# Optimization experiments

Hardware: AMD Instinct MI355X
Metric: run time of the kernel (lower is better)

Reference implementation:

```python
import jax, jax.numpy as jnp
import numpy as np


def _edge_softmax_by_src(e, src, n_nodes):
    # DGL edge_softmax(norm_by='src'): softmax over outgoing edges of each src node
    m = jax.ops.segment_max(e, src, num_segments=n_nodes)
    ex = jnp.exp(e - m[src])
    s = jax.ops.segment_sum(ex, src, num_segments=n_nodes)
    return ex / s[src]


def _l2norm(x):
    # F.normalize(p=2, dim=-1), eps=1e-12
    n = jnp.linalg.norm(x, axis=-1, keepdims=True)
    return x / jnp.maximum(n, 1e-12)


def setup_inputs() -> dict:
    key = jax.random.key(0)
    ks = jax.random.split(key, 16)
    N, E, D, NC = 50000, 1600000, 64, 16   # main graph nodes/edges, dim, classes
    NCL, ECL, FCL = 32, 1024, 16           # coarsened line graph: nodes=etypes
    s = 0.1
    inp = {
        "cl_h": jax.random.normal(ks[0], (NCL, FCL), jnp.float32),
        "cl_w": jax.random.normal(ks[1], (ECL,), jnp.float32),
        "cl_src": jax.random.randint(ks[2], (ECL,), 0, NCL, jnp.int32),
        "cl_dst": jax.random.randint(ks[3], (ECL,), 0, NCL, jnp.int32),
        "g_src": jax.random.randint(ks[4], (E,), 0, N, jnp.int32),
        "g_dst": jax.random.randint(ks[5], (E,), 0, N, jnp.int32),
        "g_etype": jax.random.randint(ks[6], (E,), 0, NCL, jnp.int32),
        # learned parameters
        "feats_emb": jax.random.normal(ks[7], (N, D), jnp.float32) * s,
        "W_e": jax.random.normal(ks[8], (FCL, D), jnp.float32) * s,      # linear_e (no bias)
        "beta1": jnp.array(1.0, jnp.float32),
        "eps1": jnp.array(0.0, jnp.float32),
        "beta2": jnp.array(1.0, jnp.float32),
        "eps2": jnp.array(0.0, jnp.float32),
        "W1a": jax.random.normal(ks[9], (D, D), jnp.float32) * s,
        "W2a": jax.random.normal(ks[10], (D, D), jnp.float32) * s,
        "W1b": jax.random.normal(ks[11], (D, D), jnp.float32) * s,
        "W2b": jax.random.normal(ks[12], (D, D), jnp.float32) * s,
        "W_pred": jax.random.normal(ks[13], (D, NC), jnp.float32) * s,
        "b_pred": jnp.zeros((NC,), jnp.float32),
    }
    return inp


def reference(cl_h, cl_w, cl_src, cl_dst, g_src, g_dst, g_etype,
              feats_emb, W_e, beta1, eps1, beta2, eps2,
              W1a, W2a, W1b, W2b, W_pred, b_pred):
    NCL = cl_h.shape[0]
    N = feats_emb.shape[0]

    def agnn(feat, beta, eps):
        p = _edge_softmax_by_src(beta * cl_w, cl_src, NCL)           # [Ecl]
        nh = _l2norm(feat)                                           # [NCL, F]
        agg = jax.ops.segment_sum(nh[cl_src] * p[:, None], cl_dst,
                                  num_segments=NCL)                  # [NCL, F]
        return (1.0 + eps) * feat + agg

    # edge-type feature propagation on coarsened line graph (dropout is eval-mode identity)
    h = jax.nn.relu(agnn(cl_h, beta1, eps1))
    h = jax.nn.relu(agnn(h, beta2, eps2))

    # per-edge relation embedding on main graph
    ew = h[g_etype] @ W_e                                            # [E, D]

    def gconv(feat, W1, W2):
        msg = feat[g_src] - ew                                       # u_sub_e, [E, D]
        agg = jax.ops.segment_sum(msg, g_dst, num_segments=N)        # [N, D]
        return jnp.tanh(feat @ W1 + agg @ W2)

    x = gconv(feats_emb, W1a, W2a)
    x = gconv(x, W1b, W2b)
    return x @ W_pred + b_pred
```

## Files before the change

### kernel.cpp

```cpp
#include <hip/hip_runtime.h>


#define TILE 8192

typedef __attribute__((ext_vector_type(8))) unsigned short us8;

__device__ __forceinline__ float b2f(unsigned short h) {
    return __uint_as_float(((unsigned)h) << 16);
}
__device__ __forceinline__ unsigned short f2b(float f) {
    const unsigned u = __float_as_uint(f);
    return (unsigned short)((u + 0x7FFFu + ((u >> 16) & 1u)) >> 16);
}

__device__ __forceinline__ unsigned ford_enc(float v) {
    unsigned b = __float_as_uint(v);
    return (b & 0x80000000u) ? ~b : (b | 0x80000000u);
}
__device__ __forceinline__ float ford_dec(unsigned k) {
    return __uint_as_float((k & 0x80000000u) ? (k ^ 0x80000000u) : ~k);
}

__global__ __launch_bounds__(512) void agnn_kernel(
    const float* __restrict__ cl_h, const float* __restrict__ cl_w,
    const int* __restrict__ cl_src, const int* __restrict__ cl_dst,
    const float* __restrict__ W_e,
    const float* __restrict__ pb1, const float* __restrict__ pe1,
    const float* __restrict__ pb2, const float* __restrict__ pe2,
    float* __restrict__ hW, int* __restrict__ bcnt, int ECL)
{
    __shared__ float w_s[1024];
    __shared__ int   src_s[1024];
    __shared__ int   dst_s[1024];
    __shared__ float h[32][16];
    __shared__ float nh[32][16];
    __shared__ float p[1024];
    __shared__ float red[32][16];
    __shared__ float acc16[32][16][16];
    __shared__ unsigned mI[32];
    __shared__ float m[32], ssum[32], nrm[32];
    const int tid = threadIdx.x;
    const int seg = tid >> 4, j = tid & 15;

    if (tid < 256) bcnt[tid] = 0;

    for (int e = tid; e < ECL; e += 512) {
        w_s[e] = cl_w[e]; src_s[e] = cl_src[e]; dst_s[e] = cl_dst[e];
    }
    h[tid >> 4][tid & 15] = cl_h[tid];
    __syncthreads();

    for (int layer = 0; layer < 2; ++layer) {
        const float beta = layer ? *pb2 : *pb1;
        const float eps  = layer ? *pe2 : *pe1;

        if (tid < 32) mI[tid] = ford_enc(-3.4e38f);
        __syncthreads();
        for (int e = tid; e < ECL; e += 512)
            atomicMax(&mI[src_s[e]], ford_enc(beta * w_s[e]));
        __syncthreads();
        if (tid < 32) m[tid] = ford_dec(mI[tid]);
        __syncthreads();

        for (int e = tid; e < ECL; e += 512)
            p[e] = __expf(beta * w_s[e] - m[src_s[e]]);
        __syncthreads();

        {
            float s = 0.f;
            #pragma unroll 4
            for (int e = j; e < ECL; e += 16)
                s += (src_s[e] == seg) ? p[e] : 0.f;
            red[seg][j] = s;
        }
        __syncthreads();
        if (tid < 32) {
            float s = 0.f;
            #pragma unroll
            for (int k = 0; k < 16; ++k) s += red[tid][k];
            ssum[tid] = s;
            float q = 0.f;
            #pragma unroll
            for (int f = 0; f < 16; ++f) { float v = h[tid][f]; q += v * v; }
            nrm[tid] = fmaxf(sqrtf(q), 1e-12f);
        }
        __syncthreads();
        for (int e = tid; e < ECL; e += 512)
            p[e] = p[e] / ssum[src_s[e]];
        nh[tid >> 4][tid & 15] = h[tid >> 4][tid & 15] / nrm[tid >> 4];
        __syncthreads();

        {
            float facc[16];
            #pragma unroll
            for (int f = 0; f < 16; ++f) facc[f] = 0.f;
            #pragma unroll 4
            for (int e = j; e < ECL; e += 16) {
                if (dst_s[e] == seg) {
                    const float pe = p[e];
                    const float4* nhrow = reinterpret_cast<const float4*>(&nh[src_s[e]][0]);
                    const float4 a0 = nhrow[0], a1 = nhrow[1], a2 = nhrow[2], a3 = nhrow[3];
                    facc[0] += pe * a0.x; facc[1] += pe * a0.y; facc[2] += pe * a0.z; facc[3] += pe * a0.w;
                    facc[4] += pe * a1.x; facc[5] += pe * a1.y; facc[6] += pe * a1.z; facc[7] += pe * a1.w;
                    facc[8] += pe * a2.x; facc[9] += pe * a2.y; facc[10] += pe * a2.z; facc[11] += pe * a2.w;
                    facc[12] += pe * a3.x; facc[13] += pe * a3.y; facc[14] += pe * a3.z; facc[15] += pe * a3.w;
                }
            }
            #pragma unroll
            for (int f = 0; f < 16; ++f) acc16[seg][j][f] = facc[f];
        }
        __syncthreads();
        {
            const int t = tid >> 4, f = tid & 15;
            float a = 0.f;
            #pragma unroll
            for (int k = 0; k < 16; ++k) a += acc16[t][k][f];
            float v = (1.f + eps) * h[t][f] + a;
            h[t][f] = fmaxf(v, 0.f);
        }
        __syncthreads();
    }

    for (int o = tid; o < 2048; o += 512) {
        const int t = o >> 6, d = o & 63;
        float s = 0.f;
        #pragma unroll
        for (int f = 0; f < 16; ++f) s += h[t][f] * W_e[f * 64 + d];
        hW[o] = s;
    }
}

__global__ __launch_bounds__(256) void tobf16_kernel(
    const float* __restrict__ x, unsigned short* __restrict__ y, int total8)
{
    const int i = blockIdx.x * 256 + threadIdx.x;
    if (i >= total8) return;
    const int base = i * 8;
    const float4 a = *reinterpret_cast<const float4*>(&x[base]);
    const float4 b = *reinterpret_cast<const float4*>(&x[base + 4]);
    us8 o;
    o[0] = f2b(a.x); o[1] = f2b(a.y); o[2] = f2b(a.z); o[3] = f2b(a.w);
    o[4] = f2b(b.x); o[5] = f2b(b.y); o[6] = f2b(b.z); o[7] = f2b(b.w);
    *reinterpret_cast<us8*>(&y[base]) = o;
}

__global__ __launch_bounds__(256) void bucket_count(
    const int* __restrict__ dst, int* __restrict__ bcnt, int E)
{
    __shared__ int lh[256];
    const int tid = threadIdx.x;
    lh[tid] = 0;
    __syncthreads();
    const int base = blockIdx.x * TILE;
    #pragma unroll
    for (int it = 0; it < 8; ++it) {
        const int i = base + (it * 256 + tid) * 4;
        if (i + 3 < E) {
            const int4 d = *reinterpret_cast<const int4*>(&dst[i]);
            atomicAdd(&lh[d.x >> 8], 1); atomicAdd(&lh[d.y >> 8], 1);
            atomicAdd(&lh[d.z >> 8], 1); atomicAdd(&lh[d.w >> 8], 1);
        } else {
            for (int k = i; k < E && k < i + 4; ++k) atomicAdd(&lh[dst[k] >> 8], 1);
        }
    }
    __syncthreads();
    if (lh[tid]) atomicAdd(&bcnt[tid], lh[tid]);
}

__global__ __launch_bounds__(256) void bucket_scan(
    const int* __restrict__ bcnt, int* __restrict__ bbase, int* __restrict__ bcur)
{
    __shared__ int ws[4];
    const int tid = threadIdx.x, lane = tid & 63, wv = tid >> 6;
    const int v = bcnt[tid];
    int x = v;
    #pragma unroll
    for (int s = 1; s < 64; s <<= 1) { const int t = __shfl_up(x, s, 64); if (lane >= s) x += t; }
    if (lane == 63) ws[wv] = x;
    __syncthreads();
    if (tid == 0) { int a = ws[0]; ws[0] = 0; for (int k = 1; k < 4; ++k) { const int b = ws[k]; ws[k] = a; a += b; } }
    __syncthreads();
    const int excl = ws[wv] + x - v;
    bbase[tid] = excl; bcur[tid] = excl;
    if (tid == 255) bbase[256] = excl + v;
}

__global__ __launch_bounds__(256) void bucket_scatter(
    const int* __restrict__ src, const int* __restrict__ dst, const int* __restrict__ et,
    int* __restrict__ bcur, unsigned* __restrict__ etmp, int E)
{
    __shared__ int lh[256], lofs[256], lcur[256], gbase[256];
    __shared__ int ws[4];
    __shared__ unsigned stage[TILE];
    __shared__ unsigned char sbk[TILE];
    const int tid = threadIdx.x, lane = tid & 63, wv = tid >> 6;
    lh[tid] = 0;
    __syncthreads();
    const int base = blockIdx.x * TILE;
    #pragma unroll
    for (int it = 0; it < 8; ++it) {
        const int i = base + (it * 256 + tid) * 4;
        if (i + 3 < E) {
            const int4 d = *reinterpret_cast<const int4*>(&dst[i]);
            atomicAdd(&lh[d.x >> 8], 1); atomicAdd(&lh[d.y >> 8], 1);
            atomicAdd(&lh[d.z >> 8], 1); atomicAdd(&lh[d.w >> 8], 1);
        } else {
            for (int k = i; k < E && k < i + 4; ++k) atomicAdd(&lh[dst[k] >> 8], 1);
        }
    }
    __syncthreads();
    {
        const int v = lh[tid];
        int x = v;
        #pragma unroll
        for (int s = 1; s < 64; s <<= 1) { const int t = __shfl_up(x, s, 64); if (lane >= s) x += t; }
        if (lane == 63) ws[wv] = x;
        __syncthreads();
        if (tid == 0) { int a = ws[0]; ws[0] = 0; for (int k = 1; k < 4; ++k) { const int b = ws[k]; ws[k] = a; a += b; } }
        __syncthreads();
        const int excl = ws[wv] + x - v;
        lofs[tid] = excl; lcur[tid] = excl;
        if (v) gbase[tid] = atomicAdd(&bcur[tid], v);
    }
    __syncthreads();
    #pragma unroll
    for (int it = 0; it < 8; ++it) {
        const int i = base + (it * 256 + tid) * 4;
        if (i + 3 < E) {
            const int4 d  = *reinterpret_cast<const int4*>(&dst[i]);
            const int4 s4 = *reinterpret_cast<const int4*>(&src[i]);
            const int4 t4 = *reinterpret_cast<const int4*>(&et[i]);
            int b, r;
            b = d.x >> 8; r = atomicAdd(&lcur[b], 1);
            stage[r] = (unsigned)s4.x | ((unsigned)(d.x & 255) << 16) | ((unsigned)t4.x << 24); sbk[r] = (unsigned char)b;
            b = d.y >> 8; r = atomicAdd(&lcur[b], 1);
            stage[r] = (unsigned)s4.y | ((unsigned)(d.y & 255) << 16) | ((unsigned)t4.y << 24); sbk[r] = (unsigned char)b;
            b = d.z >> 8; r = atomicAdd(&lcur[b], 1);
            stage[r] = (unsigned)s4.z | ((unsigned)(d.z & 255) << 16) | ((unsigned)t4.z << 24); sbk[r] = (unsigned char)b;
            b = d.w >> 8; r = atomicAdd(&lcur[b], 1);
            stage[r] = (unsigned)s4.w | ((unsigned)(d.w & 255) << 16) | ((unsigned)t4.w << 24); sbk[r] = (unsigned char)b;
        } else {
            for (int k = i; k < E && k < i + 4; ++k) {
                const int b = dst[k] >> 8;
                const int r = atomicAdd(&lcur[b], 1);
                stage[r] = (unsigned)src[k] | ((unsigned)(dst[k] & 255) << 16) | ((unsigned)et[k] << 24);
                sbk[r] = (unsigned char)b;
            }
        }
    }
    __syncthreads();
    const int tot = lofs[255] + lh[255];
    for (int i = tid; i < tot; i += 256) {
        const int b = sbk[i];
        etmp[gbase[b] + (i - lofs[b])] = stage[i];
    }
}

__global__ __launch_bounds__(256) void csr_kernel(
    const unsigned* __restrict__ etmp, const int* __restrict__ bbase,
    int* __restrict__ off, unsigned* __restrict__ ssrc, int N, int NB)
{
    __shared__ int lh[256], lofs[256], lcur[256];
    __shared__ int ws[4];
    const int tid = threadIdx.x, lane = tid & 63, wv = tid >> 6;
    const int b = blockIdx.x;
    const int s = bbase[b], e = bbase[b + 1];
    lh[tid] = 0;
    __syncthreads();
    for (int i = s + tid; i < e; i += 256)
        atomicAdd(&lh[(etmp[i] >> 16) & 255], 1);
    __syncthreads();
    {
        const int v = lh[tid];
        int x = v;
        #pragma unroll
        for (int ss = 1; ss < 64; ss <<= 1) { const int t = __shfl_up(x, ss, 64); if (lane >= ss) x += t; }
        if (lane == 63) ws[wv] = x;
        __syncthreads();
        if (tid == 0) { int a = ws[0]; ws[0] = 0; for (int k = 1; k < 4; ++k) { const int c = ws[k]; ws[k] = a; a += c; } }
        __syncthreads();
        const int excl = ws[wv] + x - v;
        lofs[tid] = excl; lcur[tid] = excl;
    }
    __syncthreads();
    const int n0 = b << 8;
    if (n0 + tid < N) off[n0 + tid] = s + lofs[tid];
    if (b == NB - 1 && tid == 0) off[N] = e;
    for (int i = s + tid; i < e; i += 256) {
        const unsigned pp = etmp[i];
        const int dl = (pp >> 16) & 255;
        const int r = atomicAdd(&lcur[dl], 1);
        ssrc[s + r] = pp;
    }
}

__global__ __launch_bounds__(256) void spmm_kernel(
    const unsigned short* __restrict__ fb, const float* __restrict__ hW,
    const int* __restrict__ off, const unsigned* __restrict__ ssrc,
    float* __restrict__ aggF, int N)
{
    __shared__ float hWl[2048];
    for (int i = threadIdx.x; i < 2048; i += 256) hWl[i] = hW[i];
    __syncthreads();
    const int lane = threadIdx.x & 63;
    const int n = blockIdx.x * 4 + (threadIdx.x >> 6);
    if (n >= N) return;
    const int half = lane >> 5, c = lane & 31;
    const int beg = off[n], end = off[n + 1];
    float a0 = 0.f, a1 = 0.f;
    int i = beg + half;
    for (; i + 14 < end; i += 16) {
        unsigned pp[8];
        #pragma unroll
        for (int jj = 0; jj < 8; ++jj) pp[jj] = ssrc[i + 2 * jj];
        unsigned u[8];
        #pragma unroll
        for (int jj = 0; jj < 8; ++jj)
            u[jj] = *reinterpret_cast<const unsigned*>(
                &fb[(size_t)(pp[jj] & 0xFFFFu) * 64 + 2 * c]);
        #pragma unroll
        for (int jj = 0; jj < 8; ++jj) {
            const float2 hw = *reinterpret_cast<const float2*>(
                &hWl[(pp[jj] >> 24) * 64 + 2 * c]);
            a0 += b2f((unsigned short)(u[jj] & 0xFFFFu)) - hw.x;
            a1 += b2f((unsigned short)(u[jj] >> 16)) - hw.y;
        }
    }
    for (; i + 6 < end; i += 8) {
        unsigned pp[4];
        #pragma unroll
        for (int jj = 0; jj < 4; ++jj) pp[jj] = ssrc[i + 2 * jj];
        unsigned u[4];
        #pragma unroll
        for (int jj = 0; jj < 4; ++jj)
            u[jj] = *reinterpret_cast<const unsigned*>(
                &fb[(size_t)(pp[jj] & 0xFFFFu) * 64 + 2 * c]);
        #pragma unroll
        for (int jj = 0; jj < 4; ++jj) {
            const float2 hw = *reinterpret_cast<const float2*>(
                &hWl[(pp[jj] >> 24) * 64 + 2 * c]);
            a0 += b2f((unsigned short)(u[jj] & 0xFFFFu)) - hw.x;
            a1 += b2f((unsigned short)(u[jj] >> 16)) - hw.y;
        }
    }
    for (; i < end; i += 2) {
        const unsigned pp = ssrc[i];
        const unsigned u = *reinterpret_cast<const unsigned*>(
            &fb[(size_t)(pp & 0xFFFFu) * 64 + 2 * c]);
        const float2 hw = *reinterpret_cast<const float2*>(
            &hWl[(pp >> 24) * 64 + 2 * c]);
        a0 += b2f((unsigned short)(u & 0xFFFFu)) - hw.x;
        a1 += b2f((unsigned short)(u >> 16)) - hw.y;
    }
    a0 += __shfl_xor(a0, 32);
    a1 += __shfl_xor(a1, 32);
    if (half == 0)
        *reinterpret_cast<float2*>(&aggF[(size_t)n * 64 + 2 * c]) = make_float2(a0, a1);
}

__global__ __launch_bounds__(256) void gconv_kernel(
    const float* __restrict__ Xf, const float* __restrict__ Af,
    const float* __restrict__ W1, const float* __restrict__ W2,
    float* __restrict__ x1f, unsigned short* __restrict__ out16,
    float* __restrict__ outf, int N, int final_mode,
    const float* __restrict__ Wp, const float* __restrict__ bp)
{
    __shared__ float4 fav[64 * 32];
    __shared__ float4 Wl[128 * 16];
    const int tid = threadIdx.x;
    const int ng = tid & 15, og = tid >> 4;
    const int n0 = blockIdx.x * 64;
    const int nb = ng * 4;

    #pragma unroll
    for (int q = 0; q < 8; ++q) {
        const int idx = q * 256 + tid;
        Wl[idx] = (idx < 1024)
            ? reinterpret_cast<const float4*>(W1)[idx]
            : reinterpret_cast<const float4*>(W2)[idx - 1024];
    }
    #pragma unroll
    for (int q = 0; q < 8; ++q) {
        const int cch = q * 256 + tid;
        const int row = cch >> 5, p = cch & 31;
        const int rn = n0 + row;
        float4 v = make_float4(0.f, 0.f, 0.f, 0.f);
        if (rn < N)
            v = (p < 16) ? reinterpret_cast<const float4*>(Xf)[(size_t)rn * 16 + p]
                         : reinterpret_cast<const float4*>(Af)[(size_t)rn * 16 + (p - 16)];
        fav[row * 32 + (p ^ ((row >> 2) & 7))] = v;
    }
    __syncthreads();

    float acc[4][4];
    #pragma unroll
    for (int i = 0; i < 4; ++i)
        #pragma unroll
        for (int j = 0; j < 4; ++j) acc[i][j] = 0.f;

    const int swz = ng & 7;
    #pragma unroll 2
    for (int kc = 0; kc < 32; ++kc) {
        const int pc = kc ^ swz;
        const float4 a0 = fav[(nb + 0) * 32 + pc];
        const float4 a1 = fav[(nb + 1) * 32 + pc];
        const float4 a2 = fav[(nb + 2) * 32 + pc];
        const float4 a3 = fav[(nb + 3) * 32 + pc];
        const float4 w0 = Wl[(kc * 4 + 0) * 16 + og];
        const float4 w1 = Wl[(kc * 4 + 1) * 16 + og];
        const float4 w2 = Wl[(kc * 4 + 2) * 16 + og];
        const float4 w3 = Wl[(kc * 4 + 3) * 16 + og];
        #pragma unroll
        for (int i = 0; i < 4; ++i) {
            const float4 a = (i == 0) ? a0 : (i == 1) ? a1 : (i == 2) ? a2 : a3;
            acc[i][0] += a.x * w0.x + a.y * w1.x + a.z * w2.x + a.w * w3.x;
            acc[i][1] += a.x * w0.y + a.y * w1.y + a.z * w2.y + a.w * w3.y;
            acc[i][2] += a.x * w0.z + a.y * w1.z + a.z * w2.z + a.w * w3.z;
            acc[i][3] += a.x * w0.w + a.y * w1.w + a.z * w2.w + a.w * w3.w;
        }
    }

    #pragma unroll
    for (int i = 0; i < 4; ++i)
        #pragma unroll
        for (int j = 0; j < 4; ++j) {
            const float e2 = __expf(2.f * acc[i][j]);
            acc[i][j] = 1.f - 2.f / (e2 + 1.f);
        }

    if (!final_mode) {
        #pragma unroll
        for (int i = 0; i < 4; ++i) {
            const int node = n0 + nb + i;
            if (node < N) {
                *reinterpret_cast<float4*>(&x1f[(size_t)node * 64 + og * 4]) =
                    make_float4(acc[i][0], acc[i][1], acc[i][2], acc[i][3]);
                const unsigned long long pk =
                    (unsigned long long)f2b(acc[i][0]) |
                    ((unsigned long long)f2b(acc[i][1]) << 16) |
                    ((unsigned long long)f2b(acc[i][2]) << 32) |
                    ((unsigned long long)f2b(acc[i][3]) << 48);
                *reinterpret_cast<unsigned long long*>(&out16[(size_t)node * 64 + og * 4]) = pk;
            }
        }
    } else {
        float* TL = reinterpret_cast<float*>(fav);
        __syncthreads();
        #pragma unroll
        for (int i = 0; i < 4; ++i)
            #pragma unroll
            for (int j = 0; j < 4; ++j)
                TL[(nb + i) * 65 + og * 4 + j] = acc[i][j];
        __syncthreads();
        const int l = tid & 63, cg = (tid >> 6) * 4;
        float o0 = bp[cg], o1 = bp[cg + 1], o2 = bp[cg + 2], o3 = bp[cg + 3];
        for (int d = 0; d < 64; ++d) {
            const float tv = TL[l * 65 + d];
            const float4 wp = *reinterpret_cast<const float4*>(&Wp[d * 16 + cg]);
            o0 += tv * wp.x; o1 += tv * wp.y; o2 += tv * wp.z; o3 += tv * wp.w;
        }
        const int node = n0 + l;
        if (node < N)
            *reinterpret_cast<float4*>(&outf[(size_t)node * 16 + cg]) =
                make_float4(o0, o1, o2, o3);
    }
}

extern "C" void kernel_launch(void* const* d_in, const int* in_sizes, int n_in,
                              void* d_out, int out_size, void* d_ws, size_t ws_size,
                              hipStream_t stream)
{
    const float* cl_h   = (const float*)d_in[0];
    const float* cl_w   = (const float*)d_in[1];
    const int*   cl_src = (const int*)d_in[2];
    const int*   cl_dst = (const int*)d_in[3];
    const int*   g_src  = (const int*)d_in[4];
    const int*   g_dst  = (const int*)d_in[5];
    const int*   g_et   = (const int*)d_in[6];
    const float* feats  = (const float*)d_in[7];
    const float* W_e    = (const float*)d_in[8];
    const float* b1     = (const float*)d_in[9];
    const float* e1     = (const float*)d_in[10];
    const float* b2     = (const float*)d_in[11];
    const float* e2     = (const float*)d_in[12];
    const float* W1a    = (const float*)d_in[13];
    const float* W2a    = (const float*)d_in[14];
    const float* W1b    = (const float*)d_in[15];
    const float* W2b    = (const float*)d_in[16];
    const float* Wp     = (const float*)d_in[17];
    const float* bp     = (const float*)d_in[18];
    const int ECL = in_sizes[1];
    const int E   = in_sizes[4];
    const int N   = in_sizes[7] / 64;
    const int NB  = (N + 255) >> 8;

    char* w = (char*)d_ws;
    auto carve = [&](size_t bytes) {
        char* r = w;
        w += (bytes + 255) & ~(size_t)255;
        return r;
    };
    float*          hW    = (float*)carve(32 * 64 * sizeof(float));
    int*            off   = (int*)carve((size_t)(N + 1) * sizeof(int));
    int*            bcnt  = (int*)carve(256 * sizeof(int));
    int*            bbase = (int*)carve(257 * sizeof(int));
    int*            bcur  = (int*)carve(256 * sizeof(int));
    unsigned*       etmp  = (unsigned*)carve((size_t)E * sizeof(unsigned));
    unsigned*       ssrc  = (unsigned*)carve((size_t)E * sizeof(unsigned));
    unsigned short* fb16  = (unsigned short*)carve((size_t)N * 64 * sizeof(unsigned short));
    unsigned short* x16   = (unsigned short*)carve((size_t)N * 64 * sizeof(unsigned short));
    float*          aggF  = (float*)carve((size_t)N * 64 * sizeof(float));
    float*          x1f   = (float*)carve((size_t)N * 64 * sizeof(float));

    const int nblk = (E + TILE - 1) / TILE;
    const int total8 = N * 8;

    agnn_kernel<<<1, 512, 0, stream>>>(cl_h, cl_w, cl_src, cl_dst, W_e,
                                       b1, e1, b2, e2, hW, bcnt, ECL);
    tobf16_kernel<<<(total8 + 255) / 256, 256, 0, stream>>>(feats, fb16, total8);
    bucket_count<<<nblk, 256, 0, stream>>>(g_dst, bcnt, E);
    bucket_scan<<<1, 256, 0, stream>>>(bcnt, bbase, bcur);
    bucket_scatter<<<nblk, 256, 0, stream>>>(g_src, g_dst, g_et, bcur, etmp, E);
    csr_kernel<<<NB, 256, 0, stream>>>(etmp, bbase, off, ssrc, N, NB);
    spmm_kernel<<<(N + 3) / 4, 256, 0, stream>>>(fb16, hW, off, ssrc, aggF, N);
    gconv_kernel<<<(N + 63) / 64, 256, 0, stream>>>(feats, aggF, W1a, W2a,
                                                    x1f, x16, nullptr, N, 0, Wp, bp);
    spmm_kernel<<<(N + 3) / 4, 256, 0, stream>>>(x16, hW, off, ssrc, aggF, N);
    gconv_kernel<<<(N + 63) / 64, 256, 0, stream>>>(x1f, aggF, W1b, W2b,
                                                    nullptr, nullptr, (float*)d_out, N, 1, Wp, bp);
}
```

Baseline: 221.0 us.

## Fuse SpMM aggregation into gconv kernel, keeping aggregates in shared memory

Merges the per-node gather/aggregate (spmm) step into the dense gconv kernel. Each 64-node block first computes its neighbour aggregates into shared memory, then runs the W1/W2 matmul and tanh. This drops the global aggF round trip and two kernel launches per layer. In exchange, the grid shrinks from N/4 blocks to N/64 blocks, each wave processes 16 nodes serially, and shared memory per block grows, which may reduce latency hiding for the irregular gathers.

```diff
diff --git a/kernel.cpp b/kernel.cpp
--- a/kernel.cpp
+++ b/kernel.cpp
@@ -294,83 +294,21 @@
     }
 }
 
-__global__ __launch_bounds__(256) void spmm_kernel(
-    const unsigned short* __restrict__ fb, const float* __restrict__ hW,
+__global__ __launch_bounds__(256) void fused_layer(
+    const unsigned short* __restrict__ gsrc,
+    const float* __restrict__ Xf,
+    const float* __restrict__ hW,
     const int* __restrict__ off, const unsigned* __restrict__ ssrc,
-    float* __restrict__ aggF, int N)
-{
-    __shared__ float hWl[2048];
-    for (int i = threadIdx.x; i < 2048; i += 256) hWl[i] = hW[i];
-    __syncthreads();
-    const int lane = threadIdx.x & 63;
-    const int n = blockIdx.x * 4 + (threadIdx.x >> 6);
-    if (n >= N) return;
-    const int half = lane >> 5, c = lane & 31;
-    const int beg = off[n], end = off[n + 1];
-    float a0 = 0.f, a1 = 0.f;
-    int i = beg + half;
-    for (; i + 14 < end; i += 16) {
-        unsigned pp[8];
-        #pragma unroll
-        for (int jj = 0; jj < 8; ++jj) pp[jj] = ssrc[i + 2 * jj];
-        unsigned u[8];
-        #pragma unroll
-        for (int jj = 0; jj < 8; ++jj)
-            u[jj] = *reinterpret_cast<const unsigned*>(
-                &fb[(size_t)(pp[jj] & 0xFFFFu) * 64 + 2 * c]);
-        #pragma unroll
-        for (int jj = 0; jj < 8; ++jj) {
-            const float2 hw = *reinterpret_cast<const float2*>(
-                &hWl[(pp[jj] >> 24) * 64 + 2 * c]);
-            a0 += b2f((unsigned short)(u[jj] & 0xFFFFu)) - hw.x;
-            a1 += b2f((unsigned short)(u[jj] >> 16)) - hw.y;
-        }
-    }
-    for (; i + 6 < end; i += 8) {
-        unsigned pp[4];
-        #pragma unroll
-        for (int jj = 0; jj < 4; ++jj) pp[jj] = ssrc[i + 2 * jj];
-        unsigned u[4];
-        #pragma unroll
-        for (int jj = 0; jj < 4; ++jj)
-            u[jj] = *reinterpret_cast<const unsigned*>(
-                &fb[(size_t)(pp[jj] & 0xFFFFu) * 64 + 2 * c]);
-        #pragma unroll
-        for (int jj = 0; jj < 4; ++jj) {
-            const float2 hw = *reinterpret_cast<const float2*>(
-                &hWl[(pp[jj] >> 24) * 64 + 2 * c]);
-            a0 += b2f((unsigned short)(u[jj] & 0xFFFFu)) - hw.x;
-            a1 += b2f((unsigned short)(u[jj] >> 16)) - hw.y;
-        }
-    }
-    for (; i < end; i += 2) {
-        const unsigned pp = ssrc[i];
-        const unsigned u = *reinterpret_cast<const unsigned*>(
-            &fb[(size_t)(pp & 0xFFFFu) * 64 + 2 * c]);
-        const float2 hw = *reinterpret_cast<const float2*>(
-            &hWl[(pp >> 24) * 64 + 2 * c]);
-        a0 += b2f((unsigned short)(u & 0xFFFFu)) - hw.x;
-        a1 += b2f((unsigned short)(u >> 16)) - hw.y;
-    }
-    a0 += __shfl_xor(a0, 32);
-    a1 += __shfl_xor(a1, 32);
-    if (half == 0)
-        *reinterpret_cast<float2*>(&aggF[(size_t)n * 64 + 2 * c]) = make_float2(a0, a1);
-}
-
-__global__ __launch_bounds__(256) void gconv_kernel(
-    const float* __restrict__ Xf, const float* __restrict__ Af,
     const float* __restrict__ W1, const float* __restrict__ W2,
-    float* __restrict__ x1f, unsigned short* __restrict__ out16,
+    float* __restrict__ x1f_out, unsigned short* __restrict__ out16,
     float* __restrict__ outf, int N, int final_mode,
     const float* __restrict__ Wp, const float* __restrict__ bp)
 {
     __shared__ float4 fav[64 * 32];
     __shared__ float4 Wl[128 * 16];
+    __shared__ float  hWl[2048];
     const int tid = threadIdx.x;
-    const int ng = tid & 15, og = tid >> 4;
     const int n0 = blockIdx.x * 64;
-    const int nb = ng * 4;
 
     #pragma unroll
     for (int q = 0; q < 8; ++q) {
@@ -380,17 +318,86 @@
             : reinterpret_cast<const float4*>(W2)[idx - 1024];
     }
     #pragma unroll
-    for (int q = 0; q < 8; ++q) {
+    for (int q = 0; q < 4; ++q) {
         const int cch = q * 256 + tid;
-        const int row = cch >> 5, p = cch & 31;
+        const int row = cch >> 4, p = cch & 15;
         const int rn = n0 + row;
         float4 v = make_float4(0.f, 0.f, 0.f, 0.f);
-        if (rn < N)
-            v = (p < 16) ? reinterpret_cast<const float4*>(Xf)[(size_t)rn * 16 + p]
-                         : reinterpret_cast<const float4*>(Af)[(size_t)rn * 16 + (p - 16)];
+        if (rn < N) v = reinterpret_cast<const float4*>(Xf)[(size_t)rn * 16 + p];
         fav[row * 32 + (p ^ ((row >> 2) & 7))] = v;
     }
-    __syncthreads();
+    #pragma unroll
+    for (int q = 0; q < 8; ++q) hWl[q * 256 + tid] = hW[q * 256 + tid];
+    __syncthreads();
+
+    {
+        const int w = tid >> 6, lane = tid & 63;
+        const int half = lane >> 5, c = lane & 31;
+        for (int i = 0; i < 16; ++i) {
+            const int nl = w * 16 + i;
+            const int n = n0 + nl;
+            float a0 = 0.f, a1 = 0.f;
+            if (n < N) {
+                const int beg = off[n], end = off[n + 1];
+                int e = beg + half;
+                for (; e + 14 < end; e += 16) {
+                    unsigned pp[8];
+                    #pragma unroll
+                    for (int jj = 0; jj < 8; ++jj) pp[jj] = ssrc[e + 2 * jj];
+                    unsigned u[8];
+                    #pragma unroll
+                    for (int jj = 0; jj < 8; ++jj)
+                        u[jj] = *reinterpret_cast<const unsigned*>(
+                            &gsrc[(size_t)(pp[jj] & 0xFFFFu) * 64 + 2 * c]);
+                    #pragma unroll
+                    for (int jj = 0; jj < 8; ++jj) {
+                        const float2 hw = *reinterpret_cast<const float2*>(
+                            &hWl[(pp[jj] >> 24) * 64 + 2 * c]);
+                        a0 += b2f((unsigned short)(u[jj] & 0xFFFFu)) - hw.x;
+                        a1 += b2f((unsigned short)(u[jj] >> 16)) - hw.y;
+                    }
+                }
+                for (; e + 6 < end; e += 8) {
+                    unsigned pp[4];
+                    #pragma unroll
+                    for (int jj = 0; jj < 4; ++jj) pp[jj] = ssrc[e + 2 * jj];
+                    unsigned u[4];
+                    #pragma unroll
+                    for (int jj = 0; jj < 4; ++jj)
+                        u[jj] = *reinterpret_cast<const unsigned*>(
+                            &gsrc[(size_t)(pp[jj] & 0xFFFFu) * 64 + 2 * c]);
+                    #pragma unroll
+                    for (int jj = 0; jj < 4; ++jj) {
+                        const float2 hw = *reinterpret_cast<const float2*>(
+                            &hWl[(pp[jj] >> 24) * 64 + 2 * c]);
+                        a0 += b2f((unsigned short)(u[jj] & 0xFFFFu)) - hw.x;
+                        a1 += b2f((unsigned short)(u[jj] >> 16)) - hw.y;
+                    }
+                }
+                for (; e < end; e += 2) {
+                    const unsigned pp = ssrc[e];
+                    const unsigned u = *reinterpret_cast<const unsigned*>(
+                        &gsrc[(size_t)(pp & 0xFFFFu) * 64 + 2 * c]);
+                    const float2 hw = *reinterpret_cast<const float2*>(
+                        &hWl[(pp >> 24) * 64 + 2 * c]);
+                    a0 += b2f((unsigned short)(u & 0xFFFFu)) - hw.x;
+                    a1 += b2f((unsigned short)(u >> 16)) - hw.y;
+                }
+            }
+            a0 += __shfl_xor(a0, 32);
+            a1 += __shfl_xor(a1, 32);
+            if (half == 0) {
+                const int chunk = 16 + (c >> 1);
+                float* d = reinterpret_cast<float*>(
+                    &fav[nl * 32 + (chunk ^ ((nl >> 2) & 7))]) + (c & 1) * 2;
+                d[0] = a0; d[1] = a1;
+            }
+        }
+    }
+    __syncthreads();
+
+    const int ng = tid & 15, og = tid >> 4;
+    const int nb = ng * 4;
 
     float acc[4][4];
     #pragma unroll
@@ -433,7 +440,7 @@
         for (int i = 0; i < 4; ++i) {
             const int node = n0 + nb + i;
             if (node < N) {
-                *reinterpret_cast<float4*>(&x1f[(size_t)node * 64 + og * 4]) =
+                *reinterpret_cast<float4*>(&x1f_out[(size_t)node * 64 + og * 4]) =
                     make_float4(acc[i][0], acc[i][1], acc[i][2], acc[i][3]);
                 const unsigned long long pk =
                     (unsigned long long)f2b(acc[i][0]) |
@@ -509,7 +516,6 @@
     unsigned*       ssrc  = (unsigned*)carve((size_t)E * sizeof(unsigned));
     unsigned short* fb16  = (unsigned short*)carve((size_t)N * 64 * sizeof(unsigned short));
     unsigned short* x16   = (unsigned short*)carve((size_t)N * 64 * sizeof(unsigned short));
-    float*          aggF  = (float*)carve((size_t)N * 64 * sizeof(float));
     float*          x1f   = (float*)carve((size_t)N * 64 * sizeof(float));
 
     const int nblk = (E + TILE - 1) / TILE;
@@ -522,10 +528,10 @@
     bucket_scan<<<1, 256, 0, stream>>>(bcnt, bbase, bcur);
     bucket_scatter<<<nblk, 256, 0, stream>>>(g_src, g_dst, g_et, bcur, etmp, E);
     csr_kernel<<<NB, 256, 0, stream>>>(etmp, bbase, off, ssrc, N, NB);
-    spmm_kernel<<<(N + 3) / 4, 256, 0, stream>>>(fb16, hW, off, ssrc, aggF, N);
-    gconv_kernel<<<(N + 63) / 64, 256, 0, stream>>>(feats, aggF, W1a, W2a,
-                                                    x1f, x16, nullptr, N, 0, Wp, bp);
-    spmm_kernel<<<(N + 3) / 4, 256, 0, stream>>>(x16, hW, off, ssrc, aggF, N);
-    gconv_kernel<<<(N + 63) / 64, 256, 0, stream>>>(x1f, aggF, W1b, W2b,
-                                                    nullptr, nullptr, (float*)d_out, N, 1, Wp, bp);
-}
+    fused_layer<<<(N + 63) / 64, 256, 0, stream>>>(fb16, feats, hW, off, ssrc,
+                                                   W1a, W2a, x1f, x16, nullptr,
+                                                   N, 0, Wp, bp);
+    fused_layer<<<(N + 63) / 64, 256, 0, stream>>>(x16, x1f, hW, off, ssrc,
+                                                   W1b, W2b, nullptr, nullptr,
+                                                   (float*)d_out, N, 1, Wp, bp);
+}
```

Result: slower. 321.6 us (+45.6%).

## Factor edge-embedding subtraction into per-node etype counts times precomputed hW·W2

Applied to the files above, without the earlier changes.

Splits the aggregated edge term algebraically: sum over incoming edges of hW[etype] becomes per-node etype counts (32 per node, built in the CSR kernel) multiplied by a precomputed -hW·W2 table. The SpMM then only gathers source features, which removes the per-edge shared-memory lookup and subtraction, and its main loop is unrolled to 16 edges. The cost is a new N×32 float count buffer and a K dimension of 160 instead of 128 in the gconv GEMM. The CSR kernel also needs 32 KB of extra shared memory for the counts.

```diff
diff --git a/kernel.cpp b/kernel.cpp
--- a/kernel.cpp
+++ b/kernel.cpp
@@ -27,7 +27,9 @@
     const float* __restrict__ W_e,
     const float* __restrict__ pb1, const float* __restrict__ pe1,
     const float* __restrict__ pb2, const float* __restrict__ pe2,
-    float* __restrict__ hW, int* __restrict__ bcnt, int ECL)
+    const float* __restrict__ W2a, const float* __restrict__ W2b,
+    float* __restrict__ nh2a, float* __restrict__ nh2b,
+    int* __restrict__ bcnt, int ECL)
 {
     __shared__ float w_s[1024];
     __shared__ int   src_s[1024];
@@ -37,6 +39,7 @@
     __shared__ float p[1024];
     __shared__ float red[32][16];
     __shared__ float acc16[32][16][16];
+    __shared__ float hWs[2048];
     __shared__ unsigned mI[32];
     __shared__ float m[32], ssum[32], nrm[32];
     const int tid = threadIdx.x;
@@ -126,7 +129,20 @@
         float s = 0.f;
         #pragma unroll
         for (int f = 0; f < 16; ++f) s += h[t][f] * W_e[f * 64 + d];
-        hW[o] = s;
+        hWs[o] = s;
+    }
+    __syncthreads();
+    for (int o = tid; o < 2048; o += 512) {
+        const int t = o >> 6, d = o & 63;
+        float sa = 0.f, sb = 0.f;
+        #pragma unroll 8
+        for (int k = 0; k < 64; ++k) {
+            const float hv = hWs[t * 64 + k];
+            sa += hv * W2a[k * 64 + d];
+            sb += hv * W2b[k * 64 + d];
+        }
+        nh2a[o] = -sa;
+        nh2b[o] = -sb;
     }
 }
 
@@ -258,17 +274,24 @@
 
 __global__ __launch_bounds__(256) void csr_kernel(
     const unsigned* __restrict__ etmp, const int* __restrict__ bbase,
-    int* __restrict__ off, unsigned* __restrict__ ssrc, int N, int NB)
+    int* __restrict__ off, unsigned* __restrict__ ssrc,
+    float* __restrict__ cntf, int N, int NB)
 {
     __shared__ int lh[256], lofs[256], lcur[256];
+    __shared__ int lcnt[8192];
     __shared__ int ws[4];
     const int tid = threadIdx.x, lane = tid & 63, wv = tid >> 6;
     const int b = blockIdx.x;
     const int s = bbase[b], e = bbase[b + 1];
     lh[tid] = 0;
-    __syncthreads();
-    for (int i = s + tid; i < e; i += 256)
-        atomicAdd(&lh[(etmp[i] >> 16) & 255], 1);
+    for (int o = tid; o < 8192; o += 256) lcnt[o] = 0;
+    __syncthreads();
+    for (int i = s + tid; i < e; i += 256) {
+        const unsigned pp = etmp[i];
+        const int dl = (pp >> 16) & 255;
+        atomicAdd(&lh[dl], 1);
+        atomicAdd(&lcnt[dl * 32 + (pp >> 24)], 1);
+    }
     __syncthreads();
     {
         const int v = lh[tid];
@@ -292,16 +315,16 @@
         const int r = atomicAdd(&lcur[dl], 1);
         ssrc[s + r] = pp;
     }
+    for (int o = tid; o < 8192; o += 256) {
+        const int node = n0 + (o >> 5);
+        if (node < N) cntf[(size_t)node * 32 + (o & 31)] = (float)lcnt[o];
+    }
 }
 
 __global__ __launch_bounds__(256) void spmm_kernel(
-    const unsigned short* __restrict__ fb, const float* __restrict__ hW,
-    const int* __restrict__ off, const unsigned* __restrict__ ssrc,
-    float* __restrict__ aggF, int N)
-{
-    __shared__ float hWl[2048];
-    for (int i = threadIdx.x; i < 2048; i += 256) hWl[i] = hW[i];
-    __syncthreads();
+    const unsigned short* __restrict__ fb, const int* __restrict__ off,
+    const unsigned* __restrict__ ssrc, float* __restrict__ aggF, int N)
+{
     const int lane = threadIdx.x & 63;
     const int n = blockIdx.x * 4 + (threadIdx.x >> 6);
     if (n >= N) return;
@@ -309,21 +332,19 @@
     const int beg = off[n], end = off[n + 1];
     float a0 = 0.f, a1 = 0.f;
     int i = beg + half;
-    for (; i + 14 < end; i += 16) {
-        unsigned pp[8];
-        #pragma unroll
-        for (int jj = 0; jj < 8; ++jj) pp[jj] = ssrc[i + 2 * jj];
-        unsigned u[8];
-        #pragma unroll
-        for (int jj = 0; jj < 8; ++jj)
+    for (; i + 30 < end; i += 32) {
+        unsigned pp[16];
+        #pragma unroll
+        for (int jj = 0; jj < 16; ++jj) pp[jj] = ssrc[i + 2 * jj];
+        unsigned u[16];
+        #pragma unroll
+        for (int jj = 0; jj < 16; ++jj)
             u[jj] = *reinterpret_cast<const unsigned*>(
                 &fb[(size_t)(pp[jj] & 0xFFFFu) * 64 + 2 * c]);
         #pragma unroll
-        for (int jj = 0; jj < 8; ++jj) {
-            const float2 hw = *reinterpret_cast<const float2*>(
-                &hWl[(pp[jj] >> 24) * 64 + 2 * c]);
-            a0 += b2f((unsigned short)(u[jj] & 0xFFFFu)) - hw.x;
-            a1 += b2f((unsigned short)(u[jj] >> 16)) - hw.y;
+        for (int jj = 0; jj < 16; ++jj) {
+            a0 += b2f((unsigned short)(u[jj] & 0xFFFFu));
+            a1 += b2f((unsigned short)(u[jj] >> 16));
         }
     }
     for (; i + 6 < end; i += 8) {
@@ -337,20 +358,16 @@
                 &fb[(size_t)(pp[jj] & 0xFFFFu) * 64 + 2 * c]);
         #pragma unroll
         for (int jj = 0; jj < 4; ++jj) {
-            const float2 hw = *reinterpret_cast<const float2*>(
-                &hWl[(pp[jj] >> 24) * 64 + 2 * c]);
-            a0 += b2f((unsigned short)(u[jj] & 0xFFFFu)) - hw.x;
-            a1 += b2f((unsigned short)(u[jj] >> 16)) - hw.y;
+            a0 += b2f((unsigned short)(u[jj] & 0xFFFFu));
+            a1 += b2f((unsigned short)(u[jj] >> 16));
         }
     }
     for (; i < end; i += 2) {
         const unsigned pp = ssrc[i];
         const unsigned u = *reinterpret_cast<const unsigned*>(
             &fb[(size_t)(pp & 0xFFFFu) * 64 + 2 * c]);
-        const float2 hw = *reinterpret_cast<const float2*>(
-            &hWl[(pp >> 24) * 64 + 2 * c]);
-        a0 += b2f((unsigned short)(u & 0xFFFFu)) - hw.x;
-        a1 += b2f((unsigned short)(u >> 16)) - hw.y;
+        a0 += b2f((unsigned short)(u & 0xFFFFu));
+        a1 += b2f((unsigned short)(u >> 16));
     }
     a0 += __shfl_xor(a0, 32);
     a1 += __shfl_xor(a1, 32);
@@ -360,24 +377,28 @@
 
 __global__ __launch_bounds__(256) void gconv_kernel(
     const float* __restrict__ Xf, const float* __restrict__ Af,
+    const float* __restrict__ cntf,
     const float* __restrict__ W1, const float* __restrict__ W2,
+    const float* __restrict__ nh2,
     float* __restrict__ x1f, unsigned short* __restrict__ out16,
     float* __restrict__ outf, int N, int final_mode,
     const float* __restrict__ Wp, const float* __restrict__ bp)
 {
-    __shared__ float4 fav[64 * 32];
-    __shared__ float4 Wl[128 * 16];
+    __shared__ float4 fav[64 * 40];
+    __shared__ float4 Wl[160 * 16];
     const int tid = threadIdx.x;
     const int ng = tid & 15, og = tid >> 4;
     const int n0 = blockIdx.x * 64;
     const int nb = ng * 4;
 
     #pragma unroll
-    for (int q = 0; q < 8; ++q) {
+    for (int q = 0; q < 10; ++q) {
         const int idx = q * 256 + tid;
         Wl[idx] = (idx < 1024)
             ? reinterpret_cast<const float4*>(W1)[idx]
-            : reinterpret_cast<const float4*>(W2)[idx - 1024];
+            : (idx < 2048)
+                ? reinterpret_cast<const float4*>(W2)[idx - 1024]
+                : reinterpret_cast<const float4*>(nh2)[idx - 2048];
     }
     #pragma unroll
     for (int q = 0; q < 8; ++q) {
@@ -388,7 +409,16 @@
         if (rn < N)
             v = (p < 16) ? reinterpret_cast<const float4*>(Xf)[(size_t)rn * 16 + p]
                          : reinterpret_cast<const float4*>(Af)[(size_t)rn * 16 + (p - 16)];
-        fav[row * 32 + (p ^ ((row >> 2) & 7))] = v;
+        fav[row * 40 + (p ^ ((row >> 2) & 7))] = v;
+    }
+    #pragma unroll
+    for (int q = 0; q < 2; ++q) {
+        const int cc = q * 256 + tid;
+        const int row = cc >> 3, p = 32 + (cc & 7);
+        const int rn = n0 + row;
+        float4 v = make_float4(0.f, 0.f, 0.f, 0.f);
+        if (rn < N) v = reinterpret_cast<const float4*>(cntf)[(size_t)rn * 8 + (cc & 7)];
+        fav[row * 40 + (p ^ ((row >> 2) & 7))] = v;
     }
     __syncthreads();
 
@@ -400,12 +430,12 @@
 
     const int swz = ng & 7;
     #pragma unroll 2
-    for (int kc = 0; kc < 32; ++kc) {
+    for (int kc = 0; kc < 40; ++kc) {
         const int pc = kc ^ swz;
-        const float4 a0 = fav[(nb + 0) * 32 + pc];
-        const float4 a1 = fav[(nb + 1) * 32 + pc];
-        const float4 a2 = fav[(nb + 2) * 32 + pc];
-        const float4 a3 = fav[(nb + 3) * 32 + pc];
+        const float4 a0 = fav[(nb + 0) * 40 + pc];
+        const float4 a1 = fav[(nb + 1) * 40 + pc];
+        const float4 a2 = fav[(nb + 2) * 40 + pc];
+        const float4 a3 = fav[(nb + 3) * 40 + pc];
         const float4 w0 = Wl[(kc * 4 + 0) * 16 + og];
         const float4 w1 = Wl[(kc * 4 + 1) * 16 + og];
         const float4 w2 = Wl[(kc * 4 + 2) * 16 + og];
@@ -500,7 +530,8 @@
         w += (bytes + 255) & ~(size_t)255;
         return r;
     };
-    float*          hW    = (float*)carve(32 * 64 * sizeof(float));
+    float*          nh2a  = (float*)carve(32 * 64 * sizeof(float));
+    float*          nh2b  = (float*)carve(32 * 64 * sizeof(float));
     int*            off   = (int*)carve((size_t)(N + 1) * sizeof(int));
     int*            bcnt  = (int*)carve(256 * sizeof(int));
     int*            bbase = (int*)carve(257 * sizeof(int));
@@ -511,21 +542,25 @@
     unsigned short* x16   = (unsigned short*)carve((size_t)N * 64 * sizeof(unsigned short));
     float*          aggF  = (float*)carve((size_t)N * 64 * sizeof(float));
     float*          x1f   = (float*)carve((size_t)N * 64 * sizeof(float));
+    float*          cntf  = (float*)carve((size_t)N * 32 * sizeof(float));
 
     const int nblk = (E + TILE - 1) / TILE;
     const int total8 = N * 8;
 
     agnn_kernel<<<1, 512, 0, stream>>>(cl_h, cl_w, cl_src, cl_dst, W_e,
-                                       b1, e1, b2, e2, hW, bcnt, ECL);
+                                       b1, e1, b2, e2, W2a, W2b,
+                                       nh2a, nh2b, bcnt, ECL);
     tobf16_kernel<<<(total8 + 255) / 256, 256, 0, stream>>>(feats, fb16, total8);
     bucket_count<<<nblk, 256, 0, stream>>>(g_dst, bcnt, E);
     bucket_scan<<<1, 256, 0, stream>>>(bcnt, bbase, bcur);
     bucket_scatter<<<nblk, 256, 0, stream>>>(g_src, g_dst, g_et, bcur, etmp, E);
-    csr_kernel<<<NB, 256, 0, stream>>>(etmp, bbase, off, ssrc, N, NB);
-    spmm_kernel<<<(N + 3) / 4, 256, 0, stream>>>(fb16, hW, off, ssrc, aggF, N);
-    gconv_kernel<<<(N + 63) / 64, 256, 0, stream>>>(feats, aggF, W1a, W2a,
+    csr_kernel<<<NB, 256, 0, stream>>>(etmp, bbase, off, ssrc, cntf, N, NB);
+    spmm_kernel<<<(N + 3) / 4, 256, 0, stream>>>(fb16, off, ssrc, aggF, N);
+    gconv_kernel<<<(N + 63) / 64, 256, 0, stream>>>(feats, aggF, cntf,
+                                                    W1a, W2a, nh2a,
                                                     x1f, x16, nullptr, N, 0, Wp, bp);
-    spmm_kernel<<<(N + 3) / 4, 256, 0, stream>>>(x16, hW, off, ssrc, aggF, N);
-    gconv_kernel<<<(N + 63) / 64, 256, 0, stream>>>(x1f, aggF, W1b, W2b,
+    spmm_kernel<<<(N + 3) / 4, 256, 0, stream>>>(x16, off, ssrc, aggF, N);
+    gconv_kernel<<<(N + 63) / 64, 256, 0, stream>>>(x1f, aggF, cntf,
+                                                    W1b, W2b, nh2b,
                                                     nullptr, nullptr, (float*)d_out, N, 1, Wp, bp);
 }
```

Measured after the change: 227.8 us. 1.03x slower.
